# Optimization experiments

Hardware: AMD Instinct MI355X
Metric: run time of the kernel (lower is better)

Reference implementation:

```python
import jax, jax.numpy as jnp
import numpy as np

# init_kwargs as module constants
RPN_BATCHSIZE = 256
RPN_CLOBBER_POSITIVES = False
RPN_FG_FRACTION = 0.5
RPN_POSITIVE_OVERLAP = 0.7
RPN_NEGATIVE_OVERLAP = 0.3

BATCH = 8
N_ANCHORS = 200000
N_GT = 20
IMG_H, IMG_W = 800.0, 1216.0


def _make_boxes(key, b, n, max_w, max_h):
    # boxes guaranteed strictly inside [0, W) x [0, H): x2 < 0.5W + 1 + 0.45W < W
    k1, k2, k3, k4 = jax.random.split(key, 4)
    x1 = jax.random.uniform(k1, (b, n)) * (max_w * 0.5)
    y1 = jax.random.uniform(k2, (b, n)) * (max_h * 0.5)
    x2 = x1 + 1.0 + jax.random.uniform(k3, (b, n)) * (max_w * 0.45)
    y2 = y1 + 1.0 + jax.random.uniform(k4, (b, n)) * (max_h * 0.45)
    return jnp.stack([x1, y1, x2, y2], axis=-1)


def setup_inputs() -> dict:
    key = jax.random.key(0)
    ka, kg, kc, ks = jax.random.split(key, 4)
    anchors = _make_boxes(ka, 1, N_ANCHORS, IMG_W, IMG_H)          # [1,N,4], all inside image
    gt_xyxy = _make_boxes(kg, BATCH, N_GT, IMG_W, IMG_H)           # [B,K,4]
    cls = jax.random.randint(kc, (BATCH, N_GT, 1), 1, 21).astype(jnp.float32)
    gt_boxes = jnp.concatenate([gt_xyxy, cls], axis=-1)            # [B,K,5]
    im_info = jnp.tile(jnp.array([[IMG_H, IMG_W, 1.0]], jnp.float32), (BATCH, 1))
    rpn_cls_score = jax.random.normal(ks, (BATCH, 18, 50, 76), jnp.float32)
    num_boxes = jnp.full((BATCH,), N_GT, jnp.int32)
    return {"rpn_cls_score": rpn_cls_score, "gt_boxes": gt_boxes,
            "im_info": im_info, "num_boxes": num_boxes, "anchors": anchors}


def bbox_overlaps_batch(anchors, gt_boxes):
    # anchors [N,4], gt_boxes [B,K,5] -> IoU overlaps [B,N,K]
    gt = gt_boxes[:, :, :4]
    gt_w = gt[:, :, 2] - gt[:, :, 0] + 1.0
    gt_h = gt[:, :, 3] - gt[:, :, 1] + 1.0
    gt_area = (gt_w * gt_h)[:, None, :]                            # [B,1,K]
    an_w = anchors[:, 2] - anchors[:, 0] + 1.0
    an_h = anchors[:, 3] - anchors[:, 1] + 1.0
    an_area = (an_w * an_h)[None, :, None]                         # [1,N,1]
    iw = (jnp.minimum(anchors[None, :, None, 2], gt[:, None, :, 2])
          - jnp.maximum(anchors[None, :, None, 0], gt[:, None, :, 0]) + 1.0)
    ih = (jnp.minimum(anchors[None, :, None, 3], gt[:, None, :, 3])
          - jnp.maximum(anchors[None, :, None, 1], gt[:, None, :, 1]) + 1.0)
    inter = jnp.maximum(iw, 0.0) * jnp.maximum(ih, 0.0)
    ov = inter / (an_area + gt_area - inter)
    gt_zero = ((gt_w == 1.0) & (gt_h == 1.0))[:, None, :]
    an_zero = ((an_w == 1.0) & (an_h == 1.0))[None, :, None]
    ov = jnp.where(gt_zero, 0.0, ov)
    ov = jnp.where(an_zero, -1.0, ov)
    return ov


def _rank_random(mask, key):
    # random rank among True positions per row (True entries get ranks 0..count-1)
    r = jax.random.uniform(key, mask.shape)
    scores = jnp.where(mask, r, 2.0)  # uniform < 1, so False entries sort last
    order = jnp.argsort(scores, axis=1)
    return jnp.argsort(order, axis=1)


def _forward(gt_boxes, anchors_all, im_info):
    B, K = gt_boxes.shape[0], gt_boxes.shape[1]
    anchors = anchors_all[0]                                       # [N,4]
    N = anchors.shape[0]
    # anchors are constructed fully inside the image (allowed_border=0), so the
    # inside-image filter keeps all anchors -> static shapes under jit
    inds_inside = jnp.arange(N)
    ov = bbox_overlaps_batch(anchors, gt_boxes)                    # [B,N,K]
    max_ov = ov.max(axis=2)                                        # [B,N]
    argmax_ov = ov.argmax(axis=2)                                  # [B,N]
    gt_max = ov.max(axis=1)                                        # [B,K]
    labels = jnp.full((B, N), -1.0, gt_boxes.dtype)
    if not RPN_CLOBBER_POSITIVES:
        labels = jnp.where(max_ov < RPN_NEGATIVE_OVERLAP, 0.0, labels)
    gt_max = jnp.where(gt_max == 0.0, 1e-5, gt_max)
    keep = (ov == gt_max[:, None, :]).sum(axis=2)                  # anchors hitting per-gt max
    labels = jnp.where(keep > 0, 1.0, labels)
    labels = jnp.where(max_ov >= RPN_POSITIVE_OVERLAP, 1.0, labels)
    if RPN_CLOBBER_POSITIVES:
        labels = jnp.where(max_ov < RPN_NEGATIVE_OVERLAP, 0.0, labels)
    # balanced fg/bg subsampling (vectorized over batch; random rank = permutation)
    num_fg = int(RPN_FG_FRACTION * RPN_BATCHSIZE)
    kfg, kbg = jax.random.split(jax.random.key(42))
    fg = labels == 1.0
    keep_fg = fg & (_rank_random(fg, kfg) < num_fg)
    labels = jnp.where(fg & ~keep_fg, -1.0, labels)
    num_bg = RPN_BATCHSIZE - keep_fg.sum(axis=1)                   # [B]
    bg = labels == 0.0
    keep_bg = bg & (_rank_random(bg, kbg) < num_bg[:, None])
    labels = jnp.where(bg & ~keep_bg, -1.0, labels)
    matches = argmax_ov + (jnp.arange(B) * K)[:, None]
    return labels, matches, inds_inside, anchors


def reference(rpn_cls_score, gt_boxes, im_info, num_boxes, anchors):
    return _forward(gt_boxes, anchors, im_info)
```

## Files before the change

kernel.cpp:

```cpp
#include <hip/hip_runtime.h>
#include <stdint.h>

#pragma clang fp contract(off)

#define BATCH 8
#define NANCH 200000
#define NGT   20
#define APT   9
#define CHUNK (256*APT)
#define PB    96
#define GRID  (PB*BATCH)
#define HBINS 1024
#define HWORDS (2*BATCH*HBINS)
#define HALF_FLAT 800000u

constexpr void ctf_round(uint32_t& x0, uint32_t& x1, int r) {
  x0 += x1; x1 = (x1 << r) | (x1 >> (32 - r)); x1 ^= x0;
}
constexpr uint64_t cenc(uint32_t k0, uint32_t k1, uint32_t x0, uint32_t x1) {
  uint32_t k2 = k0 ^ k1 ^ 0x1BD11BDAu;
  x0 += k0; x1 += k1;
  ctf_round(x0,x1,13); ctf_round(x0,x1,15); ctf_round(x0,x1,26); ctf_round(x0,x1,6);
  x0 += k1; x1 += k2 + 1u;
  ctf_round(x0,x1,17); ctf_round(x0,x1,29); ctf_round(x0,x1,16); ctf_round(x0,x1,24);
  x0 += k2; x1 += k0 + 2u;
  ctf_round(x0,x1,13); ctf_round(x0,x1,15); ctf_round(x0,x1,26); ctf_round(x0,x1,6);
  x0 += k0; x1 += k1 + 3u;
  ctf_round(x0,x1,17); ctf_round(x0,x1,29); ctf_round(x0,x1,16); ctf_round(x0,x1,24);
  x0 += k1; x1 += k2 + 4u;
  ctf_round(x0,x1,13); ctf_round(x0,x1,15); ctf_round(x0,x1,26); ctf_round(x0,x1,6);
  x0 += k2; x1 += k0 + 5u;
  return ((uint64_t)x1 << 32) | x0;
}
constexpr uint64_t EA = cenc(0u,42u,0u,2u);
constexpr uint64_t EB = cenc(0u,42u,1u,3u);
#define KF0 ((uint32_t)(EA & 0xFFFFFFFFu))
#define KF1 ((uint32_t)(EB & 0xFFFFFFFFu))
#define KG0 ((uint32_t)(EA >> 32))
#define KG1 ((uint32_t)(EB >> 32))

__device__ __forceinline__ void tf_round(uint32_t& x0, uint32_t& x1, int r) {
  x0 += x1; x1 = (x1 << r) | (x1 >> (32 - r)); x1 ^= x0;
}
__device__ __forceinline__ void threefry2x32(uint32_t k0, uint32_t k1,
                                             uint32_t x0, uint32_t x1,
                                             uint32_t& o0, uint32_t& o1) {
  uint32_t k2 = k0 ^ k1 ^ 0x1BD11BDAu;
  x0 += k0; x1 += k1;
  tf_round(x0,x1,13); tf_round(x0,x1,15); tf_round(x0,x1,26); tf_round(x0,x1,6);
  x0 += k1; x1 += k2 + 1u;
  tf_round(x0,x1,17); tf_round(x0,x1,29); tf_round(x0,x1,16); tf_round(x0,x1,24);
  x0 += k2; x1 += k0 + 2u;
  tf_round(x0,x1,13); tf_round(x0,x1,15); tf_round(x0,x1,26); tf_round(x0,x1,6);
  x0 += k0; x1 += k1 + 3u;
  tf_round(x0,x1,17); tf_round(x0,x1,29); tf_round(x0,x1,16); tf_round(x0,x1,24);
  x0 += k1; x1 += k2 + 4u;
  tf_round(x0,x1,13); tf_round(x0,x1,15); tf_round(x0,x1,26); tf_round(x0,x1,6);
  x0 += k2; x1 += k0 + 5u;
  o0 = x0; o1 = x1;
}
__device__ __forceinline__ uint32_t rbits23(uint32_t kk0, uint32_t kk1, uint32_t f) {
  uint32_t o0, o1;
  if (f < HALF_FLAT) { threefry2x32(kk0, kk1, f, f + HALF_FLAT, o0, o1); return o0 >> 9; }
  else               { threefry2x32(kk0, kk1, f - HALF_FLAT, f, o0, o1); return o1 >> 9; }
}

template<int CTRL>
__device__ __forceinline__ float dppmax(float x) {
  int xi = __float_as_int(x);
  int yi = __builtin_amdgcn_update_dpp(xi, xi, CTRL, 0xf, 0xf, false);
  return fmaxf(x, __int_as_float(yi));
}
__device__ __forceinline__ float wave_max64(float x) {
  x = dppmax<0x0B1>(x);
  x = dppmax<0x04E>(x);
  x = dppmax<0x141>(x);
  x = dppmax<0x140>(x);
  x = dppmax<0x142>(x);
  x = dppmax<0x143>(x);
  return __int_as_float(__builtin_amdgcn_readlane(__float_as_int(x), 63));
}

__global__ __launch_bounds__(256, 3)
void k_main(const float* __restrict__ gt, const float* __restrict__ anc,
            float* __restrict__ wavemax, uint32_t* __restrict__ aux,
            uint16_t* __restrict__ combo, float* __restrict__ out_matches,
            float* __restrict__ out_inds, float* __restrict__ out_anch,
            uint32_t* __restrict__ hist, int* __restrict__ gtmax_bits) {
  const int bid = blockIdx.x, t = threadIdx.x;
  const int b = bid / PB, blk = bid % PB;

  __shared__ float sx1[NGT], sy1[NGT], sx2p[NGT], sy2p[NGT], sar[NGT];
  __shared__ int   ssz[NGT];
  __shared__ int   smax[NGT];
  if (t < NGT) {
    const float* p = gt + (size_t)(b*NGT + t)*5;
    float x1=p[0], y1=p[1], x2=p[2], y2=p[3];
    float w = x2 - x1 + 1.0f, h = y2 - y1 + 1.0f;
    sx1[t]=x1; sy1[t]=y1; sx2p[t]=x2+1.0f; sy2p[t]=y2+1.0f; sar[t]=w*h;
    ssz[t] = (w==1.0f) && (h==1.0f);
    smax[t] = 0xBF800000;
  }
  __syncthreads();

  const float4* a4 = (const float4*)anc;
  const int base = blk*CHUNK + t;
  const int lane = t & 63;
  float ax[APT], ay[APT], aarea[APT], ax2p[APT], ay2p[APT];
#pragma unroll
  for (int j=0;j<APT;j++) {
    int n = base + j*256;
    if (n > NANCH-1) n = NANCH-1;
    float4 v = a4[n];
    ax[j] = v.x; ay[j] = v.y;
    float aw = v.z-v.x+1.0f, ah = v.w-v.y+1.0f;
    bool anz = (aw==1.0f)&&(ah==1.0f);
    aarea[j] = anz ? __builtin_inff() : aw*ah;
    ax2p[j] = v.z + 1.0f;
    ay2p[j] = v.w + 1.0f;
  }
  float best[APT]; int arg[APT]; uint32_t Mloc[APT];
#pragma unroll
  for (int j=0;j<APT;j++) { best[j]=-3.0f; arg[j]=0; Mloc[j]=0u; }
  float wm = 0.0f;
  for (int k=0;k<NGT;k++) {
    float ovv[APT]; float tmk;
    if (__builtin_expect(ssz[k], 0)) {
#pragma unroll
      for (int j=0;j<APT;j++) {
        ovv[j] = 0.0f;
        if (0.0f > best[j]) { best[j] = 0.0f; arg[j] = k; }
      }
      tmk = 0.0f;
    } else {
      float kx1=sx1[k], ky1=sy1[k], kx2p=sx2p[k], ky2p=sy2p[k], kar=sar[k];
      tmk = -3.0f;
#pragma unroll
      for (int j=0;j<APT;j++) {
        float iw = fminf(ax2p[j], kx2p) - fmaxf(ax[j], kx1);
        float ih = fminf(ay2p[j], ky2p) - fmaxf(ay[j], ky1);
        float inter = fmaxf(iw,0.0f)*fmaxf(ih,0.0f);
        float ov = inter * __builtin_amdgcn_rcpf((aarea[j] + kar) - inter);
        ovv[j] = ov;
        if (ov > best[j]) { best[j] = ov; arg[j] = k; }
        tmk = fmaxf(tmk, ov);
      }
    }
    const float sv = wave_max64(tmk);
#pragma unroll
    for (int j=0;j<APT;j++) if (ovv[j] == sv) Mloc[j] |= (1u<<k);
    if (lane == k)  wm = sv;
  }
  const int wid = bid*4 + (t>>6);
  if (lane < NGT) {
    wavemax[(size_t)wid*NGT + lane] = wm;
    atomicMax(&smax[lane], __float_as_int(wm));
  }
  __syncthreads();
  if (t < NGT) atomicMax(&gtmax_bits[b*NGT + t], smax[t]);
  float4* oa4 = (float4*)out_anch;
  const bool owner = (b == (blk & 7));
#pragma unroll
  for (int j=0;j<APT;j++) {
    int n = base + j*256;
    if (n >= NANCH) continue;
    uint32_t a = (Mloc[j]<<2) |
                 ((best[j] >= 0.7f) ? 2u : 0u) | ((best[j] < 0.3f) ? 1u : 0u);
    aux[(size_t)b*NANCH + n] = a;
    out_matches[(size_t)b*NANCH + n] = (float)(arg[j] + b*NGT);
    if (owner) {
      out_inds[n] = (float)n;
      oa4[n] = make_float4(ax[j], ay[j], ax2p[j]-1.0f, ay2p[j]-1.0f);
    }
    if (a & 3u) {
      uint32_t f = (uint32_t)(b*NANCH + n);
      bool isfg = (a & 2u) != 0u;
      uint32_t rb14 = rbits23(isfg?KF0:KG0, isfg?KF1:KG1, f) >> 9;
      combo[(size_t)b*NANCH + n] = (uint16_t)rb14;
      if (isfg)
        atomicAdd(&hist[b*2*HBINS + (rb14>>4)], 1u);
      else if (rb14 < HBINS)
        atomicAdd(&hist[b*2*HBINS + HBINS + rb14], 1u);
    }
  }
}

__global__ __launch_bounds__(256, 4)
void k_final(const uint32_t* __restrict__ aux, const uint16_t* __restrict__ combo,
             const float* __restrict__ wavemax, const int* __restrict__ gtmax_bits,
             const uint32_t* __restrict__ hist, float* __restrict__ out_labels) {
  const int bid = blockIdx.x, t = threadIdx.x;
  const int b = bid / PB, blk = bid % PB;
  const int lane = t & 63;
  const int w = t >> 6;
  const int wid = bid*4 + w;
  __shared__ uint32_t s_thr[2];
  __shared__ uint32_t s_fgtot;

  bool cond = false;
  if (lane < NGT) {
    float gv = __int_as_float(gtmax_bits[b*NGT + lane]);
    float rep = (gv == 0.0f) ? 1e-5f : gv;
    cond = (wavemax[(size_t)wid*NGT + lane] == rep);
  }
  uint32_t wk = (uint32_t)__ballot(cond);

  uint4 hv0, hv1, hv2, hv3;
  uint32_t mys = 0, myincl = 0;
  if (w < 2) {
    const uint4* h4 = (const uint4*)(hist + b*2*HBINS + w*HBINS + lane*16);
    hv0 = h4[0]; hv1 = h4[1]; hv2 = h4[2]; hv3 = h4[3];
    mys = hv0.x+hv0.y+hv0.z+hv0.w + hv1.x+hv1.y+hv1.z+hv1.w
        + hv2.x+hv2.y+hv2.z+hv2.w + hv3.x+hv3.y+hv3.z+hv3.w;
    uint32_t x = mys;
#pragma unroll
    for (int d=1; d<64; d<<=1) {
      uint32_t v = __shfl_up(x, d, 64);
      if (lane >= d) x += v;
    }
    myincl = x;
    if (w == 0 && lane == 63) s_fgtot = myincl;
  }
  __syncthreads();
  if (w < 2) {
    uint32_t total  = __shfl(myincl, 63, 64);
    uint32_t keptfg = (s_fgtot < 128u) ? s_fgtot : 128u;
    uint32_t target = (w == 0) ? 128u : (256u - keptfg);
    if (total <= target) {
      if (lane == 0) s_thr[w] = (w == 0) ? (HBINS-1u) : 0x3FFFu;
    } else {
      uint32_t excl = myincl - mys;
      if (excl < target && target <= myincl) {
        uint32_t bins[16] = { hv0.x,hv0.y,hv0.z,hv0.w, hv1.x,hv1.y,hv1.z,hv1.w,
                              hv2.x,hv2.y,hv2.z,hv2.w, hv3.x,hv3.y,hv3.z,hv3.w };
        uint32_t cum = excl, jj = lane*16;
        bool done = false;
#pragma unroll
        for (int i=0;i<16;i++) {
          if (!done) {
            if (cum + bins[i] >= target) { jj = lane*16 + i; done = true; }
            else cum += bins[i];
          }
        }
        s_thr[w] = jj;
      }
    }
  }
  __syncthreads();
  const uint32_t rF = s_thr[0], rB = s_thr[1];

  const int base = blk*CHUNK + t;
#pragma unroll
  for (int j=0;j<APT;j++) {
    int n = base + j*256; if (n >= NANCH) break;
    uint32_t a = aux[(size_t)b*NANCH + n];
    uint32_t rb14 = combo[(size_t)b*NANCH + n];
    uint32_t code = (a & 1u) ? 1u : 0u;
    if ((a>>2) & wk) code = 2u;
    if (a & 2u) code = 2u;
    float o = -1.0f;
    if (code == 1u) {
      o = (rb14 <= rB) ? 0.0f : -1.0f;
    } else if (code == 2u) {
      if (!(a & 2u))
        rb14 = rbits23(KF0, KF1, (uint32_t)(b*NANCH + n)) >> 9;
      o = ((rb14>>4) <= rF) ? 1.0f : -1.0f;
    }
    out_labels[(size_t)b*NANCH + n] = o;
  }
}

extern "C" void kernel_launch(void* const* d_in, const int* in_sizes, int n_in,
                              void* d_out, int out_size, void* d_ws, size_t ws_size,
                              hipStream_t stream) {
  const float* gt  = (const float*)d_in[1];
  const float* anc = (const float*)d_in[4];

  float* out         = (float*)d_out;
  float* out_labels  = out;
  float* out_matches = out + (size_t)BATCH*NANCH;
  float* out_inds    = out + (size_t)2*BATCH*NANCH;
  float* out_anch    = out_inds + NANCH;

  char* ws = (char*)d_ws;
  int*      gtmax   = (int*)(ws + 0);
  uint32_t* hist    = (uint32_t*)(ws + 1024);
  float*    wavemax = (float*)(ws + 66560);
  uint32_t* aux     = (uint32_t*)(ws + 312320);
  uint16_t* combo   = (uint16_t*)(ws + 6712320);

  (void)hipMemsetAsync(hist, 0, HWORDS*sizeof(uint32_t), stream);

  k_main <<<GRID, 256, 0, stream>>>(gt, anc, wavemax, aux, combo, out_matches,
                                    out_inds, out_anch, hist, gtmax);
  k_final<<<GRID, 256, 0, stream>>>(aux, combo, wavemax, gtmax, hist, out_labels);
}
```

Before: 113.6 us.

## Split GT loop across wave pairs and merge partial argmax via LDS

```diff
diff --git a/kernel.cpp b/kernel.cpp
--- a/kernel.cpp
+++ b/kernel.cpp
@@ -10,6 +10,7 @@
 #define CHUNK (256*APT)
 #define PB    96
 #define GRID  (PB*BATCH)
+#define NB    (GRID*2)
 #define HBINS 1024
 #define HWORDS (2*BATCH*HBINS)
 #define HALF_FLAT 800000u
@@ -81,31 +82,41 @@
   return __int_as_float(__builtin_amdgcn_readlane(__float_as_int(x), 63));
 }
 
-__global__ __launch_bounds__(256, 3)
+__global__ __launch_bounds__(256, 6)
 void k_main(const float* __restrict__ gt, const float* __restrict__ anc,
             float* __restrict__ wavemax, uint32_t* __restrict__ aux,
             uint16_t* __restrict__ combo, float* __restrict__ out_matches,
             float* __restrict__ out_inds, float* __restrict__ out_anch,
             uint32_t* __restrict__ hist, int* __restrict__ gtmax_bits) {
-  const int bid = blockIdx.x, t = threadIdx.x;
+  const int B = blockIdx.x, t = threadIdx.x;
+  const int bid = B >> 1;
   const int b = bid / PB, blk = bid % PB;
+  const int lane = t & 63;
+  const int w = t >> 6;
+  const int p = w >> 1;
+  const int h = w & 1;
+  const int w_old = 2*(B & 1) + p;
+  const int row = bid*4 + w_old;
 
   __shared__ float sx1[NGT], sy1[NGT], sx2p[NGT], sy2p[NGT], sar[NGT];
   __shared__ int   ssz[NGT];
   __shared__ int   smax[NGT];
+  __shared__ float    mbst[2][64][APT];
+  __shared__ int      marg[2][64][APT];
+  __shared__ uint32_t mml [2][64][APT];
   if (t < NGT) {
-    const float* p = gt + (size_t)(b*NGT + t)*5;
-    float x1=p[0], y1=p[1], x2=p[2], y2=p[3];
-    float w = x2 - x1 + 1.0f, h = y2 - y1 + 1.0f;
-    sx1[t]=x1; sy1[t]=y1; sx2p[t]=x2+1.0f; sy2p[t]=y2+1.0f; sar[t]=w*h;
-    ssz[t] = (w==1.0f) && (h==1.0f);
+    const float* pg = gt + (size_t)(b*NGT + t)*5;
+    float x1=pg[0], y1=pg[1], x2=pg[2], y2=pg[3];
+    float gw = x2 - x1 + 1.0f, gh = y2 - y1 + 1.0f;
+    sx1[t]=x1; sy1[t]=y1; sx2p[t]=x2+1.0f; sy2p[t]=y2+1.0f; sar[t]=gw*gh;
+    ssz[t] = (gw==1.0f) && (gh==1.0f);
     smax[t] = 0xBF800000;
   }
   __syncthreads();
 
   const float4* a4 = (const float4*)anc;
-  const int base = blk*CHUNK + t;
-  const int lane = t & 63;
+  const int t_old = 64*w_old + lane;
+  const int base = blk*CHUNK + t_old;
   float ax[APT], ay[APT], aarea[APT], ax2p[APT], ay2p[APT];
 #pragma unroll
   for (int j=0;j<APT;j++) {
@@ -123,7 +134,8 @@
 #pragma unroll
   for (int j=0;j<APT;j++) { best[j]=-3.0f; arg[j]=0; Mloc[j]=0u; }
   float wm = 0.0f;
-  for (int k=0;k<NGT;k++) {
+  for (int kk=0; kk<NGT/2; kk++) {
+    const int k = h*10 + kk;
     float ovv[APT]; float tmk;
     if (__builtin_expect(ssz[k], 0)) {
 #pragma unroll
@@ -149,15 +161,30 @@
     const float sv = wave_max64(tmk);
 #pragma unroll
     for (int j=0;j<APT;j++) if (ovv[j] == sv) Mloc[j] |= (1u<<k);
-    if (lane == k)  wm = sv;
-  }
-  const int wid = bid*4 + (t>>6);
-  if (lane < NGT) {
-    wavemax[(size_t)wid*NGT + lane] = wm;
-    atomicMax(&smax[lane], __float_as_int(wm));
+    if (lane == kk)  wm = sv;
+  }
+  if (lane < NGT/2) {
+    wavemax[(size_t)row*NGT + h*10 + lane] = wm;
+    atomicMax(&smax[h*10 + lane], __float_as_int(wm));
+  }
+  if (h == 1) {
+#pragma unroll
+    for (int j=0;j<APT;j++) {
+      mbst[p][lane][j] = best[j];
+      marg[p][lane][j] = arg[j];
+      mml [p][lane][j] = Mloc[j];
+    }
   }
   __syncthreads();
   if (t < NGT) atomicMax(&gtmax_bits[b*NGT + t], smax[t]);
+
+  if (h == 1) return;
+#pragma unroll
+  for (int j=0;j<APT;j++) {
+    float b1 = mbst[p][lane][j];
+    if (b1 > best[j]) { best[j] = b1; arg[j] = marg[p][lane][j]; }
+    Mloc[j] |= mml[p][lane][j];
+  }
   float4* oa4 = (float4*)out_anch;
   const bool owner = (b == (blk & 7));
 #pragma unroll
@@ -291,7 +318,7 @@
 
   (void)hipMemsetAsync(hist, 0, HWORDS*sizeof(uint32_t), stream);
 
-  k_main <<<GRID, 256, 0, stream>>>(gt, anc, wavemax, aux, combo, out_matches,
+  k_main <<<NB,   256, 0, stream>>>(gt, anc, wavemax, aux, combo, out_matches,
                                     out_inds, out_anch, hist, gtmax);
   k_final<<<GRID, 256, 0, stream>>>(aux, combo, wavemax, gtmax, hist, out_labels);
 }
```

Result: slower. 164.9 us (+45.1%).
